# Optimization experiments

Hardware: AMD Instinct MI355X
Metric: run time of the kernel (lower is better)

Reference implementation:

```python
import jax, jax.numpy as jnp
import numpy as np

EPS = 1e-5
NEG_SLOPE = 0.2


def _minmax(a):
    m = jnp.min(a)
    return (a - m) / (jnp.max(a) - m)


def _bn(x2d, gamma, beta):
    # train-mode BatchNorm1d: stats over axis 0 (biased variance)
    mu = x2d.mean(0)
    var = x2d.var(0)
    return gamma * (x2d - mu) * jax.lax.rsqrt(var + EPS) + beta


def _leaky(a):
    return jnp.where(a >= 0, a, NEG_SLOPE * a)


def setup_inputs() -> dict:
    key = jax.random.key(0)
    ks = jax.random.split(key, 10)
    B, C, N = 256, 1024, 80
    stdv = 1.0 / np.sqrt(C)
    return {
        "x": jax.random.normal(ks[0], (B, C, N), jnp.float32),
        "out1": jax.random.normal(ks[1], (B, N), jnp.float32),
        "adj_param": jax.random.uniform(ks[2], (N, N), jnp.float32),
        "static_weight": jax.random.uniform(ks[3], (C, C), jnp.float32, -stdv, stdv),
        "dynamic_weight": jax.random.uniform(ks[4], (C, C), jnp.float32, -stdv, stdv),
        "conv_global_w": jax.random.normal(ks[5], (C, C), jnp.float32) * 0.02,
        "conv_global_b": jnp.zeros((C,), jnp.float32),
        "conv_co_w": jax.random.normal(ks[6], (N, 2 * C), jnp.float32) * 0.02,
        "conv_co_b": jnp.zeros((N,), jnp.float32),
        "bn_gamma": jnp.ones((C,), jnp.float32),
        "bn_beta": jnp.zeros((C,), jnp.float32),
        "bng_gamma": jnp.ones((C,), jnp.float32),
        "bng_beta": jnp.zeros((C,), jnp.float32),
    }


def reference(x, out1, adj_param, static_weight, dynamic_weight,
              conv_global_w, conv_global_b, conv_co_w, conv_co_b,
              bn_gamma, bn_beta, bng_gamma, bng_beta):
    B, C, N = x.shape

    # ---- static GCN ----
    sadj = _minmax(adj_param)                               # (N,N)
    D = jax.lax.rsqrt(sadj.sum(1))                          # A.sum(1)^-0.5
    adj = D[:, None] * sadj.T * D[None, :]                  # gen_adj, diag matmuls as broadcast
    support = jnp.einsum('bcn,co->bno', x, static_weight)   # (B,N,C)
    h = jnp.einsum('nm,bmo->bno', adj, support)             # (B,N,C)
    h = _bn(h.reshape(-1, C), bn_gamma, bn_beta).reshape(B, N, C)
    out_static = _leaky(h).transpose(0, 2, 1)               # (B,C,N)
    x2 = x + out_static

    # ---- dynamic graph construction ----
    glb = x2.mean(2)                                        # GAP over nodes -> (B,C)
    glb = glb @ conv_global_w.T + conv_global_b             # 1x1 conv
    glb = _leaky(_bn(glb, bng_gamma, bng_beta))             # BN over batch (L=1)
    cat = jnp.concatenate([jnp.broadcast_to(glb[:, :, None], (B, C, N)), x2], axis=1)  # (B,2C,N)
    dadj = jnp.einsum('oc,bcn->bon', conv_co_w, cat) + conv_co_b[None, :, None]        # (B,N,N)
    dadj = _minmax(dadj)

    # ---- adjacency loss ----
    t1 = jnp.einsum('bn,bnm->bm', out1, dadj) / N
    loss = jnp.sum(jnp.linalg.norm(out1 - t1, axis=1))
    loss = loss + jnp.sum(jnp.linalg.norm((dadj - sadj).reshape(B, -1), axis=1))

    # ---- dynamic GCN ----
    Dd = jax.lax.rsqrt(dadj.sum(2))                         # (B,N)
    tadj = Dd[:, :, None] * dadj.transpose(0, 2, 1) * Dd[:, None, :]
    sup = jnp.einsum('bcn,co->bno', x2, dynamic_weight)
    h2 = jnp.einsum('bnm,bmo->bno', tadj, sup)
    h2 = _bn(h2.reshape(-1, C), bn_gamma, bn_beta).reshape(B, N, C).transpose(0, 2, 1)
    h2 = _leaky(h2)                                         # (B,C,N)
    return h2, loss
```

## Files before the change

kernel.cpp:

```cpp
#include <hip/hip_runtime.h>
#include <hip/hip_bf16.h>
#include <math.h>

#define TPB 256

constexpr int   B_  = 256;
constexpr int   C_  = 1024;
constexpr int   N_  = 80;
constexpr int   BNr = B_ * N_;
constexpr int   CN  = C_ * N_;
constexpr long  BCN = (long)B_ * C_ * N_;
constexpr int   NN  = N_ * N_;
constexpr int   BNN = B_ * NN;
constexpr float EPSf = 1e-5f;

typedef __bf16 bf16x8 __attribute__((ext_vector_type(8)));
typedef float  f32x4  __attribute__((ext_vector_type(4)));

__device__ __forceinline__ float leakyf(float v) { return v >= 0.0f ? v : 0.2f * v; }

__device__ __forceinline__ ushort f2bf(float f) {
  __hip_bfloat16 h = __float2bfloat16(f);
  ushort u; __builtin_memcpy(&u, &h, 2); return u;
}
__device__ __forceinline__ float b2f(ushort u) {
  __hip_bfloat16 h; __builtin_memcpy(&h, &u, 2);
  return __bfloat162float(h);
}

#define GLOBAL_AS __attribute__((address_space(1)))
#define LDS_AS    __attribute__((address_space(3)))
__device__ __forceinline__ void load_lds16(const void* g, void* l) {
  __builtin_amdgcn_global_load_lds((const GLOBAL_AS void*)g, (LDS_AS void*)l, 16, 0, 0);
}

__global__ __launch_bounds__(256) void k_prep_all(
    const float* __restrict__ Ws, const float* __restrict__ Wd,
    const float* __restrict__ Wco, const float* __restrict__ Wg,
    ushort* __restrict__ Wts, ushort* __restrict__ Wtd,
    ushort* __restrict__ Wco1t, ushort* __restrict__ Wco2t, ushort* __restrict__ Wg_bf,
    float* __restrict__ zbase,
    const float* __restrict__ ap, float* __restrict__ sadj,
    ushort* __restrict__ adj_bf, float* __restrict__ lossa) {
  __shared__ float sh[NN];
  __shared__ float red[TPB];
  __shared__ float sD[N_];
  __shared__ float s_lo, s_hi;
  const int t = threadIdx.x;
  const int blk = blockIdx.x;
  if (blk < 2048) {
    const float* W = (blk < 1024) ? Ws : Wd;
    ushort* Wt = (blk < 1024) ? Wts : Wtd;
    const int bb = blk & 1023;
    const int bx = bb & 31, by = bb >> 5;
    const int tx = t % 32, ty = t / 32;
    const int r0 = by * 32, c0 = bx * 32;
#pragma unroll
    for (int k = 0; k < 4; ++k) sh[(ty + 8 * k) * 33 + tx] = W[(size_t)(r0 + ty + 8 * k) * C_ + c0 + tx];
    __syncthreads();
#pragma unroll
    for (int k = 0; k < 4; ++k) Wt[(size_t)(c0 + ty + 8 * k) * C_ + r0 + tx] = f2bf(sh[tx * 33 + ty + 8 * k]);
  } else if (blk < 2208) {
    const int i4 = ((blk - 2048) * TPB + t) * 4;
    const int o = i4 >> 11, k = i4 & 2047;
    float4 v = *(const float4*)&Wco[(size_t)o * 2048 + k];
    ushort4 u;
    u.x = f2bf(v.x); u.y = f2bf(v.y); u.z = f2bf(v.z); u.w = f2bf(v.w);
    if (k < C_) *(ushort4*)&Wco1t[(size_t)o * C_ + k] = u;
    else        *(ushort4*)&Wco2t[(size_t)o * C_ + (k - C_)] = u;
  } else if (blk < 3232) {
    const long i4 = ((long)(blk - 2208) * TPB + t) * 4;
    float4 v = *(const float4*)&Wg[i4];
    ushort4 u;
    u.x = f2bf(v.x); u.y = f2bf(v.y); u.z = f2bf(v.z); u.w = f2bf(v.w);
    *(ushort4*)&Wg_bf[i4] = u;
  } else if (blk < 3258) {
    const int i = ((blk - 3232) * TPB + t) * 4;
    float4 z = make_float4(0.f, 0.f, 0.f, 0.f);
    *(float4*)&zbase[i] = z;
  } else {
    float lo = 3.4e38f, hi = -3.4e38f;
    for (int i = t; i < NN; i += TPB) { float v = ap[i]; sh[i] = v; lo = fminf(lo, v); hi = fmaxf(hi, v); }
    red[t] = lo; __syncthreads();
    for (int o = 128; o > 0; o >>= 1) { if (t < o) red[t] = fminf(red[t], red[t + o]); __syncthreads(); }
    if (t == 0) s_lo = red[0];
    __syncthreads();
    red[t] = hi; __syncthreads();
    for (int o = 128; o > 0; o >>= 1) { if (t < o) red[t] = fmaxf(red[t], red[t + o]); __syncthreads(); }
    if (t == 0) s_hi = red[0];
    __syncthreads();
    const float inv = 1.0f / (s_hi - s_lo);
    for (int i = t; i < NN; i += TPB) { float v = (sh[i] - s_lo) * inv; sh[i] = v; sadj[i] = v; }
    __syncthreads();
    if (t < N_) { float sum = 0.f; for (int m = 0; m < N_; ++m) sum += sh[t * N_ + m]; sD[t] = rsqrtf(sum); }
    if (t == 0) *lossa = 0.0f;
    __syncthreads();
    for (int i = t; i < N_ * 96; i += TPB) {
      const int n = i / 96, m = i % 96;
      adj_bf[i] = f2bf((m < N_) ? sD[n] * sh[m * N_ + n] * sD[m] : 0.0f);
    }
  }
}

__global__ __launch_bounds__(256) void k_fold_mfma(const float* __restrict__ Xf32,
                                                   const ushort* __restrict__ Xbf,
                                                   const void* __restrict__ adjsrc,
                                                   ushort* __restrict__ outp, int mode,
                                                   const float* __restrict__ bmin,
                                                   const float* __restrict__ bmax) {
  __shared__ __align__(16) ushort sX[128][104];
  __shared__ __align__(16) ushort sAdj[80][104];
  __shared__ float sD[N_];
  __shared__ float rl[TPB], rh[TPB];
  __shared__ float s_lo, s_inv;
  const int t = threadIdx.x;
  const int b  = blockIdx.x >> 3;
  const int c0 = (blockIdx.x & 7) * 128;

  if (mode == 0) {
    const ushort* ab = (const ushort*)adjsrc;
    for (int i = t; i < (N_ * 96) / 4; i += TPB) {
      ushort4 v = *(const ushort4*)&ab[i * 4];
      *(ushort4*)&sAdj[(i * 4) / 96][(i * 4) % 96] = v;
    }
    __syncthreads();
  } else {
    rl[t] = (t < 160) ? bmin[t] : 3.4e38f;
    rh[t] = (t < 160) ? bmax[t] : -3.4e38f;
    __syncthreads();
    for (int o = 128; o > 0; o >>= 1) {
      if (t < o) { rl[t] = fminf(rl[t], rl[t + o]); rh[t] = fmaxf(rh[t], rh[t + o]); }
      __syncthreads();
    }
    if (t == 0) { s_lo = rl[0]; s_inv = 1.0f / (rh[0] - rl[0]); }
    __syncthreads();
    const float lo = s_lo, inv = s_inv;
    float* sF = (float*)&sX[0][0];
    const float* db = (const float*)adjsrc + (size_t)b * NN;
    for (int i = t; i < NN / 4; i += TPB) {
      float4 v = *(const float4*)&db[i * 4];
      v.x = (v.x - lo) * inv; v.y = (v.y - lo) * inv;
      v.z = (v.z - lo) * inv; v.w = (v.w - lo) * inv;
      *(float4*)&sF[i * 4] = v;
    }
    __syncthreads();
    if (t < N_) { float s = 0.f; for (int m = 0; m < N_; ++m) s += sF[t * N_ + m]; sD[t] = rsqrtf(s); }
    __syncthreads();
    for (int i = t; i < N_ * 96; i += TPB) {
      const int n = i / 96, m = i % 96;
      sAdj[n][m] = f2bf((m < N_) ? sF[m * N_ + n] * sD[n] * sD[m] : 0.0f);
    }
    __syncthreads();
  }

  if (mode == 0) {
    const float* Xb = Xf32 + ((size_t)b * C_ + c0) * N_;
    for (int i = t; i < (128 * N_) / 4; i += TPB) {
      float4 v = *(const float4*)&Xb[i * 4];
      const int r = (i * 4) / N_, m = (i * 4) % N_;
      ushort4 u; u.x = f2bf(v.x); u.y = f2bf(v.y); u.z = f2bf(v.z); u.w = f2bf(v.w);
      *(ushort4*)&sX[r][m] = u;
    }
  } else {
    const ushort* Xb = Xbf + ((size_t)b * C_ + c0) * N_;
    for (int i = t; i < (128 * N_) / 8; i += TPB) {
      const int r = i / 10, m = (i % 10) * 8;
      uint4 v = *(const uint4*)&Xb[(size_t)r * N_ + m];
      *(uint4*)&sX[r][m] = v;
    }
  }
  for (int i = t; i < (128 * 16) / 4; i += TPB) {
    const int r = i / 4, m = 80 + (i % 4) * 4;
    ushort4 z; z.x = 0; z.y = 0; z.z = 0; z.w = 0;
    *(ushort4*)&sX[r][m] = z;
  }
  __syncthreads();

  const int lane = t & 63, wid = t >> 6;
  const int l16 = lane & 15, lq = lane >> 4;
  f32x4 acc[2][5];
#pragma unroll
  for (int i = 0; i < 2; ++i)
#pragma unroll
    for (int j = 0; j < 5; ++j) { f32x4 z = {0.f, 0.f, 0.f, 0.f}; acc[i][j] = z; }
  bf16x8 af[2][3], bfr[5][3];
#pragma unroll
  for (int i = 0; i < 2; ++i)
#pragma unroll
    for (int kk = 0; kk < 3; ++kk)
      af[i][kk] = *(const bf16x8*)&sX[wid * 32 + i * 16 + l16][kk * 32 + lq * 8];
#pragma unroll
  for (int j = 0; j < 5; ++j)
#pragma unroll
    for (int kk = 0; kk < 3; ++kk)
      bfr[j][kk] = *(const bf16x8*)&sAdj[j * 16 + l16][kk * 32 + lq * 8];
#pragma unroll
  for (int i = 0; i < 2; ++i)
#pragma unroll
    for (int j = 0; j < 5; ++j)
#pragma unroll
      for (int kk = 0; kk < 3; ++kk)
        acc[i][j] = __builtin_amdgcn_mfma_f32_16x16x32_bf16(af[i][kk], bfr[j][kk], acc[i][j], 0, 0, 0);

  ushort* ob = outp + (size_t)b * CN;
#pragma unroll
  for (int i = 0; i < 2; ++i) {
    const int c = c0 + wid * 32 + i * 16 + lq * 4;
#pragma unroll
    for (int j = 0; j < 5; ++j) {
      const int n = j * 16 + l16;
      ushort4 u;
      u.x = f2bf(acc[i][j][0]); u.y = f2bf(acc[i][j][1]);
      u.z = f2bf(acc[i][j][2]); u.w = f2bf(acc[i][j][3]);
      *(ushort4*)&ob[(size_t)n * C_ + c] = u;
    }
  }
}

__global__ __launch_bounds__(512, 2) void k_gemm_320(const ushort* __restrict__ A,
                                                     const ushort* __restrict__ Bt,
                                                     void* __restrict__ outp, int out_bf,
                                                     float* __restrict__ bnsum,
                                                     float* __restrict__ bnsq) {
  __shared__ ushort sA[2][320 * 64];
  __shared__ ushort sB[2][128 * 64];
  const int t = threadIdx.x;
  const int lane = t & 63, wid = t >> 6;
  const int wm = wid >> 1, wn = wid & 1;
  const int l16 = lane & 15, lq = lane >> 4;

  const int lin = blockIdx.x;
  const int xcd = lin & 7, bi = lin >> 3;
  const int tm = xcd * 8 + (bi >> 3);
  const int tn = bi & 7;
  const int m0 = tm * 320, o0 = tn * 128;

  const int srow = t >> 3;
  const int sswz = ((t & 7) ^ ((t >> 3) & 7)) * 8;

  f32x4 acc[5][4];
#pragma unroll
  for (int i = 0; i < 5; ++i)
#pragma unroll
    for (int j = 0; j < 4; ++j) { f32x4 z = {0.f, 0.f, 0.f, 0.f}; acc[i][j] = z; }

#define STA(PAR, ROWB, KT) load_lds16(A  + (size_t)(m0 + (ROWB) + srow) * C_ + (KT) * 64 + sswz, \
                                      &sA[PAR][((ROWB) + (wid << 3)) * 64])
#define STB(PAR, ROWB, KT) load_lds16(Bt + (size_t)(o0 + (ROWB) + srow) * C_ + (KT) * 64 + sswz, \
                                      &sB[PAR][((ROWB) + (wid << 3)) * 64])
#define STAGE_T(PAR, KT) { STA(PAR, 0, KT); STA(PAR, 64, KT); STA(PAR, 128, KT); \
                           STA(PAR, 192, KT); STA(PAR, 256, KT); \
                           STB(PAR, 0, KT); STB(PAR, 64, KT); }

#define PH(PAR, KK, STAGES, VMW)                                                          \
  {                                                                                       \
    STAGES                                                                                \
    bf16x8 afr[5], bfr[4];                                                                \
    _Pragma("unroll") for (int fi = 0; fi < 5; ++fi)                                      \
      afr[fi] = *(const bf16x8*)&sA[PAR][(wm * 80 + fi * 16 + l16) * 64 +                 \
                                         (((KK) * 4 + lq) ^ (l16 & 7)) * 8];              \
    _Pragma("unroll") for (int gi = 0; gi < 4; ++gi)                                      \
      bfr[gi] = *(const bf16x8*)&sB[PAR][(wn * 64 + gi * 16 + l16) * 64 +                 \
                                         (((KK) * 4 + lq) ^ (l16 & 7)) * 8];              \
    asm volatile("s_barrier" ::: "memory");                                               \
    asm volatile("s_waitcnt lgkmcnt(0)" ::: "memory");                                    \
    __builtin_amdgcn_s_setprio(1);                                                        \
    _Pragma("unroll") for (int fi = 0; fi < 5; ++fi)                                      \
      _Pragma("unroll") for (int gi = 0; gi < 4; ++gi)                                    \
        acc[fi][gi] = __builtin_amdgcn_mfma_f32_16x16x32_bf16(afr[fi], bfr[gi],           \
                                                              acc[fi][gi], 0, 0, 0);      \
    __builtin_amdgcn_s_setprio(0);                                                        \
    VMW                                                                                   \
    asm volatile("s_barrier" ::: "memory");                                               \
  }

  STAGE_T(0, 0);
  asm volatile("s_waitcnt vmcnt(0)" ::: "memory");
  asm volatile("s_barrier" ::: "memory");

  for (int i = 0; i < 8; ++i) {
    const int t1 = 2 * i + 1, t2 = 2 * i + 2;
    PH(0, 0, { STAGE_T(1, t1); }, {})
    PH(0, 1, {}, { asm volatile("s_waitcnt vmcnt(0)" ::: "memory"); })
    PH(1, 0, { if (i < 7) STAGE_T(0, t2); }, {})
    PH(1, 1, {}, { if (i < 7) { asm volatile("s_waitcnt vmcnt(0)" ::: "memory"); } })
  }

#pragma unroll
  for (int fi = 0; fi < 5; ++fi) {
    const int mg = m0 + wm * 80 + fi * 16 + lq * 4;
    const int b  = mg / 80;
    const int n0 = mg - b * 80;
#pragma unroll
    for (int gi = 0; gi < 4; ++gi) {
      const int og = o0 + wn * 64 + gi * 16 + l16;
      const size_t off = (size_t)b * CN + (size_t)og * N_ + n0;
      if (out_bf) {
        ushort4 u;
        u.x = f2bf(acc[fi][gi][0]); u.y = f2bf(acc[fi][gi][1]);
        u.z = f2bf(acc[fi][gi][2]); u.w = f2bf(acc[fi][gi][3]);
        *(ushort4*)((ushort*)outp + off) = u;
      } else {
        *(f32x4*)((float*)outp + off) = acc[fi][gi];
      }
    }
  }

  {
    float* redS = (float*)&sA[0][0];
    float* redQ = redS + 2048;
    const int slot = wm * 4 + lq;
#pragma unroll
    for (int gi = 0; gi < 4; ++gi) {
      float s = 0.f, q = 0.f;
#pragma unroll
      for (int fi = 0; fi < 5; ++fi)
#pragma unroll
        for (int r = 0; r < 4; ++r) { const float v = acc[fi][gi][r]; s += v; q += v * v; }
      const int ol = wn * 64 + gi * 16 + l16;
      redS[ol * 16 + slot] = s;
      redQ[ol * 16 + slot] = q;
    }
    __syncthreads();
    if (t < 128) {
      float s = 0.f, q = 0.f;
#pragma unroll
      for (int k = 0; k < 16; ++k) { s += redS[t * 16 + k]; q += redQ[t * 16 + k]; }
      atomicAdd(&bnsum[o0 + t], s);
      atomicAdd(&bnsq[o0 + t], q);
    }
  }
#undef STA
#undef STB
#undef STAGE_T
#undef PH
}

__global__ __launch_bounds__(256) void k_dadj_mfma(const ushort* __restrict__ A,
                                                   const ushort* __restrict__ Bw,
                                                   const float* __restrict__ go,
                                                   const float* __restrict__ bco,
                                                   float* __restrict__ dadj,
                                                   float* __restrict__ bmin,
                                                   float* __restrict__ bmax) {
  __shared__ ushort smA[128 * 32];
  __shared__ ushort smB[80 * 32];
  const int t = threadIdx.x;
  const int lane = t & 63, wid = t >> 6;
  const int m0 = blockIdx.x * 128;
  const int rto = t >> 2, ch = t & 3;
  const size_t gA0 = (size_t)(m0 + rto) * C_ + (size_t)ch * 8;
  ushort* ldsA = smA + wid * 512;
  const int l16 = lane & 15, lq = lane >> 4;
  const int wrow = wid * 32;
  f32x4 zero = {0.f, 0.f, 0.f, 0.f};
  f32x4 acc[2][5];
#pragma unroll
  for (int i = 0; i < 2; ++i)
#pragma unroll
    for (int j = 0; j < 5; ++j) acc[i][j] = zero;
  for (int k0 = 0; k0 < C_; k0 += 32) {
    load_lds16(A + gA0 + k0,            ldsA);
    load_lds16(A + gA0 + 64 * C_ + k0,  ldsA + 2048);
    {
      const int idx = t;
      uint4 v = *(const uint4*)&Bw[(size_t)(idx >> 2) * C_ + k0 + (idx & 3) * 8];
      *(uint4*)&smB[idx * 8] = v;
      if (t < 64) {
        const int idx2 = 256 + t;
        uint4 v2 = *(const uint4*)&Bw[(size_t)(idx2 >> 2) * C_ + k0 + (idx2 & 3) * 8];
        *(uint4*)&smB[idx2 * 8] = v2;
      }
    }
    __syncthreads();
    bf16x8 af[2], bfr[5];
#pragma unroll
    for (int i = 0; i < 2; ++i) af[i]  = *(const bf16x8*)&smA[(wrow + i * 16 + l16) * 32 + lq * 8];
#pragma unroll
    for (int j = 0; j < 5; ++j) bfr[j] = *(const bf16x8*)&smB[(j * 16 + l16) * 32 + lq * 8];
#pragma unroll
    for (int i = 0; i < 2; ++i)
#pragma unroll
      for (int j = 0; j < 5; ++j)
        acc[i][j] = __builtin_amdgcn_mfma_f32_16x16x32_bf16(af[i], bfr[j], acc[i][j], 0, 0, 0);
    __syncthreads();
  }
  float vlo = 3.4e38f, vhi = -3.4e38f;
#pragma unroll
  for (int i = 0; i < 2; ++i) {
    const int mg = m0 + wrow + i * 16 + lq * 4;
    const int b  = mg / 80;
    const int n0 = mg - b * 80;
    const float* gob = go + b * N_;
#pragma unroll
    for (int j = 0; j < 5; ++j) {
      const int o = j * 16 + l16;
      const float g = gob[o] + bco[o];
      f32x4 v = acc[i][j];
      v[0] += g; v[1] += g; v[2] += g; v[3] += g;
      vlo = fminf(vlo, fminf(fminf(v[0], v[1]), fminf(v[2], v[3])));
      vhi = fmaxf(vhi, fmaxf(fmaxf(v[0], v[1]), fmaxf(v[2], v[3])));
      *(f32x4*)&dadj[(size_t)b * NN + (size_t)o * N_ + n0] = v;
    }
  }
  float* red = (float*)smA;
  red[t] = vlo; red[TPB + t] = vhi;
  __syncthreads();
  for (int o = 128; o > 0; o >>= 1) {
    if (t < o) {
      red[t] = fminf(red[t], red[t + o]);
      red[TPB + t] = fmaxf(red[TPB + t], red[TPB + t + o]);
    }
    __syncthreads();
  }
  if (t == 0) { bmin[blockIdx.x] = red[0]; bmax[blockIdx.x] = red[TPB]; }
}

__global__ __launch_bounds__(256) void k_glb_mfma(const ushort* __restrict__ A,
                                                  const ushort* __restrict__ Bw,
                                                  const float* __restrict__ bias,
                                                  float* __restrict__ outp,
                                                  float* __restrict__ gsum,
                                                  float* __restrict__ gsq) {
  __shared__ ushort smA[2][64 * 32];
  __shared__ ushort smB[2][64 * 32];
  const int t = threadIdx.x;
  const int lane = t & 63, wid = t >> 6;
  const int o0 = blockIdx.x * 64, m0 = blockIdx.y * 64;
  const int rto = t >> 2, ch = t & 3;
  const size_t gA0 = (size_t)(m0 + rto) * C_ + (size_t)ch * 8;
  const size_t gB0 = (size_t)(o0 + rto) * C_ + (size_t)ch * 8;
  const int l16 = lane & 15, lq = lane >> 4;
  const int wm = wid & 1, wn = wid >> 1;
  f32x4 zero = {0.f, 0.f, 0.f, 0.f};
  f32x4 acc[2][2];
#pragma unroll
  for (int i = 0; i < 2; ++i)
#pragma unroll
    for (int j = 0; j < 2; ++j) acc[i][j] = zero;
  for (int k0 = 0; k0 < C_; k0 += 64) {
    load_lds16(A  + gA0 + k0,       smA[0] + wid * 512);
    load_lds16(A  + gA0 + k0 + 32,  smA[1] + wid * 512);
    load_lds16(Bw + gB0 + k0,       smB[0] + wid * 512);
    load_lds16(Bw + gB0 + k0 + 32,  smB[1] + wid * 512);
    __syncthreads();
#pragma unroll
    for (int h = 0; h < 2; ++h) {
      bf16x8 af[2], bfr[2];
#pragma unroll
      for (int i = 0; i < 2; ++i) af[i]  = *(const bf16x8*)&smA[h][(wm * 32 + i * 16 + l16) * 32 + lq * 8];
#pragma unroll
      for (int j = 0; j < 2; ++j) bfr[j] = *(const bf16x8*)&smB[h][(wn * 32 + j * 16 + l16) * 32 + lq * 8];
#pragma unroll
      for (int i = 0; i < 2; ++i)
#pragma unroll
        for (int j = 0; j < 2; ++j)
          acc[i][j] = __builtin_amdgcn_mfma_f32_16x16x32_bf16(af[i], bfr[j], acc[i][j], 0, 0, 0);
    }
    __syncthreads();
  }
  float ssv[2] = {0.f, 0.f}, sqv[2] = {0.f, 0.f};
#pragma unroll
  for (int i = 0; i < 2; ++i) {
    const int mg = m0 + wm * 32 + i * 16 + lq * 4;
#pragma unroll
    for (int j = 0; j < 2; ++j) {
      const int og = o0 + wn * 32 + j * 16 + l16;
      const float bs = bias[og];
      f32x4 v = acc[i][j];
#pragma unroll
      for (int r = 0; r < 4; ++r) {
        const float val = v[r] + bs;
        outp[(size_t)(mg + r) * C_ + og] = val;
        ssv[j] += val; sqv[j] += val * val;
      }
    }
  }
  {
    float* redS = (float*)&smA[0][0];
    float* redQ = redS + 512;
    const int slot = wm * 4 + lq;
#pragma unroll
    for (int j = 0; j < 2; ++j) {
      const int ol = wn * 32 + j * 16 + l16;
      redS[ol * 8 + slot] = ssv[j];
      redQ[ol * 8 + slot] = sqv[j];
    }
    __syncthreads();
    if (t < 64) {
      float s = 0.f, q = 0.f;
#pragma unroll
      for (int k = 0; k < 8; ++k) { s += redS[t * 8 + k]; q += redQ[t * 8 + k]; }
      atomicAdd(&gsum[o0 + t], s);
      atomicAdd(&gsq[o0 + t], q);
    }
  }
}

__global__ __launch_bounds__(256) void k_go_mfma(const float* __restrict__ glb1,
                                                 const ushort* __restrict__ Bw,
                                                 const float* __restrict__ gsum,
                                                 const float* __restrict__ gsq,
                                                 const float* __restrict__ gg,
                                                 const float* __restrict__ gb,
                                                 float* __restrict__ go) {
  __shared__ ushort smA[128 * 32];
  __shared__ ushort smB[80 * 32];
  __shared__ float pgm[C_], pmu[C_], pgb[C_];
  const int t = threadIdx.x;
  const int lane = t & 63, wid = t >> 6;
  const int kbase = blockIdx.x * 128;
  const int m0 = blockIdx.y * 128;
  const int rto = t >> 2, ch = t & 3;
  const int l16 = lane & 15, lq = lane >> 4;
  const int wrow = wid * 32;
  for (int c = t; c < C_; c += TPB) {
    const float mu = gsum[c] * (1.0f / B_);
    const float var = gsq[c] * (1.0f / B_) - mu * mu;
    pgm[c] = gg[c] * rsqrtf(var + EPSf); pmu[c] = mu; pgb[c] = gb[c];
  }
  __syncthreads();
  f32x4 zero = {0.f, 0.f, 0.f, 0.f};
  f32x4 acc[2][5];
#pragma unroll
  for (int i = 0; i < 2; ++i)
#pragma unroll
    for (int j = 0; j < 5; ++j) acc[i][j] = zero;
  for (int kk0 = 0; kk0 < 128; kk0 += 32) {
    const int k0 = kbase + kk0;
#pragma unroll
    for (int h = 0; h < 2; ++h) {
      const float* src = &glb1[(size_t)(m0 + h * 64 + rto) * C_ + k0 + ch * 8];
      float4 a0 = *(const float4*)src;
      float4 a1 = *(const float4*)(src + 4);
      float av[8] = {a0.x, a0.y, a0.z, a0.w, a1.x, a1.y, a1.z, a1.w};
      ushort4 u0, u1;
      const int cb = k0 + ch * 8;
      u0.x = f2bf(leakyf(pgm[cb+0]*(av[0]-pmu[cb+0])+pgb[cb+0]));
      u0.y = f2bf(leakyf(pgm[cb+1]*(av[1]-pmu[cb+1])+pgb[cb+1]));
      u0.z = f2bf(leakyf(pgm[cb+2]*(av[2]-pmu[cb+2])+pgb[cb+2]));
      u0.w = f2bf(leakyf(pgm[cb+3]*(av[3]-pmu[cb+3])+pgb[cb+3]));
      u1.x = f2bf(leakyf(pgm[cb+4]*(av[4]-pmu[cb+4])+pgb[cb+4]));
      u1.y = f2bf(leakyf(pgm[cb+5]*(av[5]-pmu[cb+5])+pgb[cb+5]));
      u1.z = f2bf(leakyf(pgm[cb+6]*(av[6]-pmu[cb+6])+pgb[cb+6]));
      u1.w = f2bf(leakyf(pgm[cb+7]*(av[7]-pmu[cb+7])+pgb[cb+7]));
      *(ushort4*)&smA[h * 2048 + t * 8]     = u0;
      *(ushort4*)&smA[h * 2048 + t * 8 + 4] = u1;
    }
    {
      const int idx = t;
      uint4 v = *(const uint4*)&Bw[(size_t)(idx >> 2) * C_ + k0 + (idx & 3) * 8];
      *(uint4*)&smB[idx * 8] = v;
      if (t < 64) {
        const int idx2 = 256 + t;
        uint4 v2 = *(const uint4*)&Bw[(size_t)(idx2 >> 2) * C_ + k0 + (idx2 & 3) * 8];
        *(uint4*)&smB[idx2 * 8] = v2;
      }
    }
    __syncthreads();
    bf16x8 af[2], bfr[5];
#pragma unroll
    for (int i = 0; i < 2; ++i) af[i]  = *(const bf16x8*)&smA[(wrow + i * 16 + l16) * 32 + lq * 8];
#pragma unroll
    for (int j = 0; j < 5; ++j) bfr[j] = *(const bf16x8*)&smB[(j * 16 + l16) * 32 + lq * 8];
#pragma unroll
    for (int i = 0; i < 2; ++i)
#pragma unroll
      for (int j = 0; j < 5; ++j)
        acc[i][j] = __builtin_amdgcn_mfma_f32_16x16x32_bf16(af[i], bfr[j], acc[i][j], 0, 0, 0);
    __syncthreads();
  }
#pragma unroll
  for (int i = 0; i < 2; ++i) {
    const int mg = m0 + wrow + i * 16 + lq * 4;
#pragma unroll
    for (int j = 0; j < 5; ++j) {
      const int o = j * 16 + l16;
#pragma unroll
      for (int r = 0; r < 4; ++r)
        atomicAdd(&go[(size_t)(mg + r) * N_ + o], acc[i][j][r]);
    }
  }
}

__global__ __launch_bounds__(256) void k_x2_fused(
    const float* __restrict__ x, ushort* __restrict__ hx,
    const float* __restrict__ g, const float* __restrict__ be,
    const float* __restrict__ ssum, const float* __restrict__ ssq,
    ushort* __restrict__ x2t, ushort* __restrict__ glb0b) {
  __shared__ float s[64][85];
  __shared__ float pg[64], pm[64], pb[64];
  const int t = threadIdx.x;
  const long row0 = (long)blockIdx.x * 64;
  const int b = (int)(row0 >> 10), c0 = (int)(row0 & 1023);
  if (t < 64) {
    const int c = c0 + t;
    const float mu = ssum[c] * (1.0f / BNr);
    const float var = ssq[c] * (1.0f / BNr) - mu * mu;
    const float rstd = rsqrtf(var + EPSf);
    pg[t] = g[c] * rstd; pm[t] = mu; pb[t] = be[c];
  }
  __syncthreads();
  const float* xb = x  + row0 * N_;
  ushort*      hb = hx + row0 * N_;
  for (int i4 = t; i4 < (64 * N_) / 4; i4 += TPB) {
    const int e = i4 * 4, r = e / N_, n = e % N_;
    float4 xv = *(const float4*)&xb[e];
    ushort4 hu = *(const ushort4*)&hb[e];
    const float gm = pg[r], m = pm[r], bb = pb[r];
    float4 o;
    o.x = xv.x + leakyf(gm * (b2f(hu.x) - m) + bb);
    o.y = xv.y + leakyf(gm * (b2f(hu.y) - m) + bb);
    o.z = xv.z + leakyf(gm * (b2f(hu.z) - m) + bb);
    o.w = xv.w + leakyf(gm * (b2f(hu.w) - m) + bb);
    *(float4*)&s[r][n] = o;
    ushort4 ou;
    ou.x = f2bf(o.x); ou.y = f2bf(o.y); ou.z = f2bf(o.z); ou.w = f2bf(o.w);
    *(ushort4*)&hb[e] = ou;
  }
  __syncthreads();
  const int tx = t % 16, ty = t / 16;
  ushort* tb = x2t + (size_t)b * CN + c0 + tx * 4;
#pragma unroll
  for (int u = 0; u < 5; ++u) {
    const int n = ty + 16 * u;
    ushort4 v;
    v.x = f2bf(s[tx * 4 + 0][n]); v.y = f2bf(s[tx * 4 + 1][n]);
    v.z = f2bf(s[tx * 4 + 2][n]); v.w = f2bf(s[tx * 4 + 3][n]);
    *(ushort4*)&tb[(size_t)n * C_] = v;
  }
  {
    const int r = t >> 2, q = t & 3;
    float sacc = 0.f;
    for (int n = q; n < N_; n += 4) sacc += s[r][n];
    sacc += __shfl_down(sacc, 1);
    sacc += __shfl_down(sacc, 2);
    if (q == 0) glb0b[(size_t)b * C_ + c0 + r] = f2bf(sacc * (1.0f / N_));
  }
}

__global__ void k_loss(const float* __restrict__ dadj, const float* __restrict__ sadj,
                       const float* __restrict__ out1, float* __restrict__ lossa,
                       const float* __restrict__ bmin, const float* __restrict__ bmax) {
  const int b = blockIdx.x, t = threadIdx.x;
  __shared__ float red[TPB], red2[TPB];
  __shared__ float slo, sinv, s2;
  red[t]  = (t < 160) ? bmin[t] : 3.4e38f;
  red2[t] = (t < 160) ? bmax[t] : -3.4e38f;
  __syncthreads();
  for (int o = 128; o > 0; o >>= 1) {
    if (t < o) { red[t] = fminf(red[t], red[t + o]); red2[t] = fmaxf(red2[t], red2[t + o]); }
    __syncthreads();
  }
  if (t == 0) { slo = red[0]; sinv = 1.0f / (red2[0] - red[0]); }
  __syncthreads();
  const float lo = slo, inv = sinv;
  const float* db = dadj + (long)b * NN;
  const float* o1 = out1 + b * N_;
  float p2 = 0.f;
  for (int i = t; i < NN; i += TPB) { const float d = (db[i] - lo) * inv - sadj[i]; p2 += d * d; }
  float p1 = 0.f;
  if (t < N_) {
    float acc = 0.f;
    for (int n = 0; n < N_; ++n) acc += o1[n] * ((db[n * N_ + t] - lo) * inv);
    const float d = o1[t] - acc * (1.0f / N_);
    p1 = d * d;
  }
  red[t] = p2; __syncthreads();
  for (int o = 128; o > 0; o >>= 1) { if (t < o) red[t] += red[t + o]; __syncthreads(); }
  if (t == 0) s2 = red[0];
  __syncthreads();
  red[t] = p1; __syncthreads();
  for (int o = 128; o > 0; o >>= 1) { if (t < o) red[t] += red[t + o]; __syncthreads(); }
  if (t == 0) atomicAdd(lossa, sqrtf(s2) + sqrtf(red[0]));
}

__global__ void k_final(const ushort* __restrict__ h2, float* __restrict__ outp,
                        const float* __restrict__ g, const float* __restrict__ be,
                        const float* __restrict__ ssum, const float* __restrict__ ssq,
                        const float* __restrict__ lossa) {
  const long i = ((long)blockIdx.x * TPB + threadIdx.x) * 4;
  const int c = (int)((i / N_) % C_);
  ushort4 hu = *(const ushort4*)&h2[i];
  const float mu = ssum[c] * (1.0f / BNr);
  const float rstd = rsqrtf(ssq[c] * (1.0f / BNr) - mu * mu + EPSf);
  const float gm = g[c] * rstd, bb = be[c];
  float4 v;
  v.x = leakyf(gm * (b2f(hu.x) - mu) + bb);
  v.y = leakyf(gm * (b2f(hu.y) - mu) + bb);
  v.z = leakyf(gm * (b2f(hu.z) - mu) + bb);
  v.w = leakyf(gm * (b2f(hu.w) - mu) + bb);
  *(float4*)&outp[i] = v;
  if (blockIdx.x == 0 && threadIdx.x == 0) outp[BCN] = *lossa;
}

extern "C" void kernel_launch(void* const* d_in, const int* in_sizes, int n_in,
                              void* d_out, int out_size, void* d_ws, size_t ws_size,
                              hipStream_t stream) {
  const float* x    = (const float*)d_in[0];
  const float* out1 = (const float*)d_in[1];
  const float* ap   = (const float*)d_in[2];
  const float* Ws   = (const float*)d_in[3];
  const float* Wd   = (const float*)d_in[4];
  const float* Wg   = (const float*)d_in[5];
  const float* bg   = (const float*)d_in[6];
  const float* Wco  = (const float*)d_in[7];
  const float* bco  = (const float*)d_in[8];
  const float* bn_g  = (const float*)d_in[9];
  const float* bn_b  = (const float*)d_in[10];
  const float* bng_g = (const float*)d_in[11];
  const float* bng_b = (const float*)d_in[12];
  float* out = (float*)d_out;

  float* w = (float*)d_ws;
  float* sadj  = w;
  float* dadj  = sadj + NN;
  float* glb0  = dadj + BNN;
  float* glb1  = glb0 + B_ * C_;
  float* go    = glb1 + B_ * C_;
  float* ssum1 = go + BNr;
  float* ssq1  = ssum1 + C_;
  float* ssum2 = ssq1 + C_;
  float* ssq2  = ssum2 + C_;
  float* gsum  = ssq2 + C_;
  float* gsq   = gsum + C_;
  float* bmin  = gsq + C_;
  float* bmax  = bmin + 512;
  float* lossa = bmax + 512;
  ushort* ub   = (ushort*)(((uintptr_t)(lossa + 1) + 255) & ~(uintptr_t)255);
  ushort* xa_bf  = ub;
  ushort* hT_bf  = xa_bf + BCN;
  ushort* Wts    = hT_bf + BCN;
  ushort* Wtd    = Wts + (size_t)C_ * C_;
  ushort* Wco2t  = Wtd + (size_t)C_ * C_;
  ushort* adj_bf = Wco2t + (size_t)N_ * C_;
  ushort* Wg_bf   = (ushort*)dadj;
  ushort* Wco1t   = (ushort*)dadj + (size_t)C_ * C_;
  ushort* glb0_bf = (ushort*)glb0;
  ushort* x2t_bf  = xa_bf;

  k_prep_all<<<3259, TPB, 0, stream>>>(Ws, Wd, Wco, Wg, Wts, Wtd, Wco1t, Wco2t, Wg_bf,
                                       go, ap, sadj, adj_bf, lossa);

  k_fold_mfma<<<B_ * 8, TPB, 0, stream>>>(x, hT_bf, adj_bf, xa_bf, 0, bmin, bmax);
  k_gemm_320<<<512, 512, 0, stream>>>(xa_bf, Wts, hT_bf, 1, ssum1, ssq1);
  k_x2_fused<<<(B_ * C_) / 64, TPB, 0, stream>>>(x, hT_bf, bn_g, bn_b, ssum1, ssq1,
                                                 x2t_bf, glb0_bf);

  k_glb_mfma<<<dim3(C_ / 64, B_ / 64), TPB, 0, stream>>>(glb0_bf, Wg_bf, bg, glb1, gsum, gsq);
  k_go_mfma<<<dim3(8, B_ / 128), TPB, 0, stream>>>(glb1, Wco1t, gsum, gsq, bng_g, bng_b, go);
  k_dadj_mfma<<<BNr / 128, TPB, 0, stream>>>(x2t_bf, Wco2t, go, bco, dadj, bmin, bmax);

  k_loss<<<B_, TPB, 0, stream>>>(dadj, sadj, out1, lossa, bmin, bmax);

  k_fold_mfma<<<B_ * 8, TPB, 0, stream>>>(x, hT_bf, dadj, xa_bf, 1, bmin, bmax);
  k_gemm_320<<<512, 512, 0, stream>>>(xa_bf, Wtd, hT_bf, 1, ssum2, ssq2);
  k_final<<<(int)(BCN / (4 * TPB)), TPB, 0, stream>>>(hT_bf, out, bn_g, bn_b, ssum2, ssq2, lossa);
}
```

Baseline: 491.4 us.

## Fuse adjacency loss into dynamic fold kernel and shrink GEMM tile to 160 rows

The separate k_loss kernel is removed. Its per-batch loss terms are now computed inside the mode-1 fold kernel, reusing the already-normalized dadj tile in shared memory, on one block out of every eight per batch. The large GEMM also moves from 512-thread, 320-row tiles to 256-thread, 160-row tiles with twice as many blocks, and the BN-statistics reduction layout is adjusted to match. This saves a kernel launch and a reread of dadj, and changes occupancy and tile shape, at the cost of less A/B reuse per block and extra serialized work in some fold blocks.

Result: faster. 467.2 us (-4.9%).

```diff
diff --git a/kernel.cpp b/kernel.cpp
--- a/kernel.cpp
+++ b/kernel.cpp
@@ -107,7 +107,10 @@
                                                    const void* __restrict__ adjsrc,
                                                    ushort* __restrict__ outp, int mode,
                                                    const float* __restrict__ bmin,
-                                                   const float* __restrict__ bmax) {
+                                                   const float* __restrict__ bmax,
+                                                   const float* __restrict__ sadj,
+                                                   const float* __restrict__ out1,
+                                                   float* __restrict__ lossa) {
   __shared__ __align__(16) ushort sX[128][104];
   __shared__ __align__(16) ushort sAdj[80][104];
   __shared__ float sD[N_];
@@ -151,6 +154,26 @@
       sAdj[n][m] = f2bf((m < N_) ? sF[m * N_ + n] * sD[n] * sD[m] : 0.0f);
     }
     __syncthreads();
+    if ((blockIdx.x & 7) == 0) {
+      const float* o1 = out1 + b * N_;
+      float p2 = 0.f;
+      for (int i = t; i < NN; i += TPB) { const float d = sF[i] - sadj[i]; p2 += d * d; }
+      float p1 = 0.f;
+      if (t < N_) {
+        float a = 0.f;
+        for (int n = 0; n < N_; ++n) a += o1[n] * sF[n * N_ + t];
+        const float d = o1[t] - a * (1.0f / N_);
+        p1 = d * d;
+      }
+      rl[t] = p2; rh[t] = p1;
+      __syncthreads();
+      for (int o = 128; o > 0; o >>= 1) {
+        if (t < o) { rl[t] += rl[t + o]; rh[t] += rh[t + o]; }
+        __syncthreads();
+      }
+      if (t == 0) atomicAdd(lossa, sqrtf(rl[0]) + sqrtf(rh[0]));
+      __syncthreads();
+    }
   }
 
   if (mode == 0) {
@@ -217,12 +240,12 @@
   }
 }
 
-__global__ __launch_bounds__(512, 2) void k_gemm_320(const ushort* __restrict__ A,
+__global__ __launch_bounds__(256, 2) void k_gemm_160(const ushort* __restrict__ A,
                                                      const ushort* __restrict__ Bt,
                                                      void* __restrict__ outp, int out_bf,
                                                      float* __restrict__ bnsum,
                                                      float* __restrict__ bnsq) {
-  __shared__ ushort sA[2][320 * 64];
+  __shared__ ushort sA[2][160 * 64];
   __shared__ ushort sB[2][128 * 64];
   const int t = threadIdx.x;
   const int lane = t & 63, wid = t >> 6;
@@ -231,9 +254,9 @@
 
   const int lin = blockIdx.x;
   const int xcd = lin & 7, bi = lin >> 3;
-  const int tm = xcd * 8 + (bi >> 3);
+  const int tm = xcd * 16 + (bi >> 3);
   const int tn = bi & 7;
-  const int m0 = tm * 320, o0 = tn * 128;
+  const int m0 = tm * 160, o0 = tn * 128;
 
   const int srow = t >> 3;
   const int sswz = ((t & 7) ^ ((t >> 3) & 7)) * 8;
@@ -248,9 +271,9 @@
                                       &sA[PAR][((ROWB) + (wid << 3)) * 64])
 #define STB(PAR, ROWB, KT) load_lds16(Bt + (size_t)(o0 + (ROWB) + srow) * C_ + (KT) * 64 + sswz, \
                                       &sB[PAR][((ROWB) + (wid << 3)) * 64])
-#define STAGE_T(PAR, KT) { STA(PAR, 0, KT); STA(PAR, 64, KT); STA(PAR, 128, KT); \
-                           STA(PAR, 192, KT); STA(PAR, 256, KT); \
-                           STB(PAR, 0, KT); STB(PAR, 64, KT); }
+#define STAGE_T(PAR, KT) { STA(PAR, 0, KT); STA(PAR, 32, KT); STA(PAR, 64, KT); \
+                           STA(PAR, 96, KT); STA(PAR, 128, KT); \
+                           STB(PAR, 0, KT); STB(PAR, 32, KT); STB(PAR, 64, KT); STB(PAR, 96, KT); }
 
 #define PH(PAR, KK, STAGES, VMW)                                                          \
   {                                                                                       \
@@ -308,7 +331,7 @@
 
   {
     float* redS = (float*)&sA[0][0];
-    float* redQ = redS + 2048;
+    float* redQ = redS + 1024;
     const int slot = wm * 4 + lq;
 #pragma unroll
     for (int gi = 0; gi < 4; ++gi) {
@@ -318,14 +341,14 @@
 #pragma unroll
         for (int r = 0; r < 4; ++r) { const float v = acc[fi][gi][r]; s += v; q += v * v; }
       const int ol = wn * 64 + gi * 16 + l16;
-      redS[ol * 16 + slot] = s;
-      redQ[ol * 16 + slot] = q;
+      redS[ol * 8 + slot] = s;
+      redQ[ol * 8 + slot] = q;
     }
     __syncthreads();
     if (t < 128) {
       float s = 0.f, q = 0.f;
 #pragma unroll
-      for (int k = 0; k < 16; ++k) { s += redS[t * 16 + k]; q += redQ[t * 16 + k]; }
+      for (int k = 0; k < 8; ++k) { s += redS[t * 8 + k]; q += redQ[t * 8 + k]; }
       atomicAdd(&bnsum[o0 + t], s);
       atomicAdd(&bnsq[o0 + t], q);
     }
@@ -637,42 +660,6 @@
     sacc += __shfl_down(sacc, 2);
     if (q == 0) glb0b[(size_t)b * C_ + c0 + r] = f2bf(sacc * (1.0f / N_));
   }
-}
-
-__global__ void k_loss(const float* __restrict__ dadj, const float* __restrict__ sadj,
-                       const float* __restrict__ out1, float* __restrict__ lossa,
-                       const float* __restrict__ bmin, const float* __restrict__ bmax) {
-  const int b = blockIdx.x, t = threadIdx.x;
-  __shared__ float red[TPB], red2[TPB];
-  __shared__ float slo, sinv, s2;
-  red[t]  = (t < 160) ? bmin[t] : 3.4e38f;
-  red2[t] = (t < 160) ? bmax[t] : -3.4e38f;
-  __syncthreads();
-  for (int o = 128; o > 0; o >>= 1) {
-    if (t < o) { red[t] = fminf(red[t], red[t + o]); red2[t] = fmaxf(red2[t], red2[t + o]); }
-    __syncthreads();
-  }
-  if (t == 0) { slo = red[0]; sinv = 1.0f / (red2[0] - red[0]); }
-  __syncthreads();
-  const float lo = slo, inv = sinv;
-  const float* db = dadj + (long)b * NN;
-  const float* o1 = out1 + b * N_;
-  float p2 = 0.f;
-  for (int i = t; i < NN; i += TPB) { const float d = (db[i] - lo) * inv - sadj[i]; p2 += d * d; }
-  float p1 = 0.f;
-  if (t < N_) {
-    float acc = 0.f;
-    for (int n = 0; n < N_; ++n) acc += o1[n] * ((db[n * N_ + t] - lo) * inv);
-    const float d = o1[t] - acc * (1.0f / N_);
-    p1 = d * d;
-  }
-  red[t] = p2; __syncthreads();
-  for (int o = 128; o > 0; o >>= 1) { if (t < o) red[t] += red[t + o]; __syncthreads(); }
-  if (t == 0) s2 = red[0];
-  __syncthreads();
-  red[t] = p1; __syncthreads();
-  for (int o = 128; o > 0; o >>= 1) { if (t < o) red[t] += red[t + o]; __syncthreads(); }
-  if (t == 0) atomicAdd(lossa, sqrtf(s2) + sqrtf(red[0]));
 }
 
 __global__ void k_final(const ushort* __restrict__ h2, float* __restrict__ outp,
@@ -742,8 +729,9 @@
   k_prep_all<<<3259, TPB, 0, stream>>>(Ws, Wd, Wco, Wg, Wts, Wtd, Wco1t, Wco2t, Wg_bf,
                                        go, ap, sadj, adj_bf, lossa);
 
-  k_fold_mfma<<<B_ * 8, TPB, 0, stream>>>(x, hT_bf, adj_bf, xa_bf, 0, bmin, bmax);
-  k_gemm_320<<<512, 512, 0, stream>>>(xa_bf, Wts, hT_bf, 1, ssum1, ssq1);
+  k_fold_mfma<<<B_ * 8, TPB, 0, stream>>>(x, hT_bf, adj_bf, xa_bf, 0, bmin, bmax,
+                                          sadj, out1, lossa);
+  k_gemm_160<<<1024, TPB, 0, stream>>>(xa_bf, Wts, hT_bf, 1, ssum1, ssq1);
   k_x2_fused<<<(B_ * C_) / 64, TPB, 0, stream>>>(x, hT_bf, bn_g, bn_b, ssum1, ssq1,
                                                  x2t_bf, glb0_bf);
 
@@ -751,9 +739,8 @@
   k_go_mfma<<<dim3(8, B_ / 128), TPB, 0, stream>>>(glb1, Wco1t, gsum, gsq, bng_g, bng_b, go);
   k_dadj_mfma<<<BNr / 128, TPB, 0, stream>>>(x2t_bf, Wco2t, go, bco, dadj, bmin, bmax);
 
-  k_loss<<<B_, TPB, 0, stream>>>(dadj, sadj, out1, lossa, bmin, bmax);
-
-  k_fold_mfma<<<B_ * 8, TPB, 0, stream>>>(x, hT_bf, dadj, xa_bf, 1, bmin, bmax);
-  k_gemm_320<<<512, 512, 0, stream>>>(xa_bf, Wtd, hT_bf, 1, ssum2, ssq2);
+  k_fold_mfma<<<B_ * 8, TPB, 0, stream>>>(x, hT_bf, dadj, xa_bf, 1, bmin, bmax,
+                                          sadj, out1, lossa);
+  k_gemm_160<<<1024, TPB, 0, stream>>>(xa_bf, Wtd, hT_bf, 1, ssum2, ssq2);
   k_final<<<(int)(BCN / (4 * TPB)), TPB, 0, stream>>>(hT_bf, out, bn_g, bn_b, ssum2, ssq2, lossa);
 }
```
